# Kernel optimization log

Hardware: AMD Instinct MI355X
Metric: run time of the kernel (lower is better)

## Reference

```python
import jax, jax.numpy as jnp
import numpy as np

DIM = 1024
NUM_HEADS = 16
HEAD_DIM = DIM // NUM_HEADS
SCALE = HEAD_DIM ** -0.5
B, N = 2, 2048


def setup_inputs() -> dict:
    key = jax.random.key(0)
    k_x, k_qkv, k_prjw, k_prjb = jax.random.split(key, 4)
    # nn.Linear(dim, 3*dim, bias=False): weight [3*dim, dim]
    s = 1.0 / np.sqrt(DIM)
    return {
        "x": jax.random.normal(k_x, (B, N, DIM), dtype=jnp.float32),
        "w_qkv": jax.random.uniform(k_qkv, (3 * DIM, DIM), jnp.float32, -s, s),
        "w_prj": jax.random.uniform(k_prjw, (DIM, DIM), jnp.float32, -s, s),
        "b_prj": jax.random.uniform(k_prjb, (DIM,), jnp.float32, -s, s),
    }


def reference(x, w_qkv, w_prj, b_prj):
    Bb, Nn, C = x.shape
    qkv = jnp.einsum("bnc,dc->bnd", x, w_qkv)            # [B,N,3C]
    qkv = qkv.reshape(Bb, Nn, 3, NUM_HEADS, HEAD_DIM)
    qkv = jnp.transpose(qkv, (2, 0, 3, 1, 4))            # [3,B,H,N,hd]
    q, k, v = qkv[0], qkv[1], qkv[2]
    attn = jnp.einsum("bhqd,bhkd->bhqk", q, k) * SCALE   # [B,H,N,N]
    attn = jax.nn.softmax(attn, axis=-1)
    out = jnp.einsum("bhqk,bhkd->bhqd", attn, v)         # [B,H,N,hd]
    out = jnp.transpose(out, (0, 2, 1, 3)).reshape(Bb, Nn, C)
    # dropout layers are identity at eval / p=0
    return jnp.einsum("bnc,dc->bnd", out, w_prj) + b_prj
```

## Files before the change

### kernel.cpp

```cpp
#include <hip/hip_runtime.h>

typedef unsigned short u16;
typedef unsigned int u32;
typedef __attribute__((ext_vector_type(8))) short s16x8;
typedef __attribute__((ext_vector_type(4))) short s16x4;
typedef __attribute__((ext_vector_type(4))) float f32x4;

#define DIM    1024
#define NHEADS 16
#define HD     64
#define NSEQ   2048
#define QKVN   3072

__device__ __forceinline__ u16 f2bf(float f) {
  u32 u = __float_as_uint(f);
  u += 0x7FFF + ((u >> 16) & 1);
  return (u16)(u >> 16);
}

__device__ __forceinline__ float vexp2(float x) {
#if __has_builtin(__builtin_amdgcn_exp2f)
  return __builtin_amdgcn_exp2f(x);
#else
  return __expf(x * 0.69314718055994531f);
#endif
}

__device__ __forceinline__ void async16(const u16* g, u16* l) {
  __builtin_amdgcn_global_load_lds(
      (const __attribute__((address_space(1))) unsigned int*)g,
      (__attribute__((address_space(3))) unsigned int*)l, 16, 0, 0);
}

__global__ void cast_all(const float* __restrict__ x, const float* __restrict__ wq,
                         const float* __restrict__ wp, u16* __restrict__ xo,
                         u16* __restrict__ wqo, u16* __restrict__ wpo) {
  int i = blockIdx.x * 256 + threadIdx.x;
  const float4* src; u16* dst; int off;
  if (i < 1048576)      { src = (const float4*)x;  dst = xo;  off = i; }
  else if (i < 1835008) { src = (const float4*)wq; dst = wqo; off = i - 1048576; }
  else                  { src = (const float4*)wp; dst = wpo; off = i - 1835008; }
  float4 f = src[off];
  ushort4 o;
  o.x = f2bf(f.x); o.y = f2bf(f.y); o.z = f2bf(f.z); o.w = f2bf(f.w);
  ((ushort4*)dst)[off] = o;
}

template <bool FINAL>
__global__ __launch_bounds__(256, 3) void gemm_bt(
    const u16* __restrict__ A, const u16* __restrict__ Bw, u16* __restrict__ qkv,
    u16* __restrict__ vt, const float* __restrict__ bias, float* __restrict__ outp) {
  constexpr int K = 1024;
  constexpr int BM = FINAL ? 64 : 128;
  constexpr int MT = FINAL ? 64 : 32;
  constexpr int IT = FINAL ? 2 : 4;
  constexpr int ACALLS = BM / 16;
  constexpr int TCALLS = ACALLS + 8;
  constexpr int PW = TCALLS / 4;
  const int bm = blockIdx.x % MT;
  const int bn = blockIdx.x / MT;
  const int tid = threadIdx.x;
  const int wave = tid >> 6, lane = tid & 63;
  const int q4 = lane >> 4, l15 = lane & 15;
  const int wm = wave >> 1, wn = wave & 1;
  const int m0 = bm * BM, n0 = bn * 128;

  __shared__ alignas(16) u16 lsA[BM * 32];
  __shared__ alignas(16) u16 lsB[128 * 32];

  f32x4 acc[IT][4];
#pragma unroll
  for (int i = 0; i < IT; i++)
#pragma unroll
    for (int j = 0; j < 4; j++) acc[i][j] = (f32x4){0.f, 0.f, 0.f, 0.f};

  for (int k0 = 0; k0 < K; k0 += 32) {
    __syncthreads();
#pragma unroll
    for (int j = 0; j < PW; ++j) {
      int t = wave * PW + j;
      if (t < ACALLS) {
        int lin = t * 64 + lane;
        int r = lin >> 2, c = lin & 3;
        async16(A + (size_t)(m0 + r) * K + k0 + c * 8, lsA + t * 512);
      } else {
        int tb = t - ACALLS;
        int lin = tb * 64 + lane;
        int r = lin >> 2, c = lin & 3;
        async16(Bw + (size_t)(n0 + r) * K + k0 + c * 8, lsB + tb * 512);
      }
    }
    __syncthreads();
    s16x8 af[IT], bfr[4];
#pragma unroll
    for (int i = 0; i < IT; ++i)
      af[i] = *(const s16x8*)(lsA + (wm * (IT * 16) + i * 16 + l15) * 32 + q4 * 8);
#pragma unroll
    for (int j = 0; j < 4; ++j)
      bfr[j] = *(const s16x8*)(lsB + (wn * 64 + j * 16 + l15) * 32 + q4 * 8);
#pragma unroll
    for (int i = 0; i < IT; ++i)
#pragma unroll
      for (int j = 0; j < 4; ++j)
        acc[i][j] = __builtin_amdgcn_mfma_f32_16x16x32_bf16(af[i], bfr[j], acc[i][j], 0, 0, 0);
  }

#pragma unroll
  for (int i = 0; i < IT; i++) {
#pragma unroll
    for (int j = 0; j < 4; j++) {
      int n = n0 + wn * 64 + j * 16 + l15;
      int mb = m0 + wm * (IT * 16) + i * 16 + q4 * 4;
      if (FINAL) {
#pragma unroll
        for (int r = 0; r < 4; r++)
          outp[(size_t)(mb + r) * DIM + n] = acc[i][j][r] + bias[n];
      } else if (n < 2048) {
#pragma unroll
        for (int r = 0; r < 4; r++)
          qkv[(size_t)(mb + r) * QKVN + n] = f2bf(acc[i][j][r]);
      } else {
        int b = mb >> 11, tok = mb & 2047;
        int h = (n >> 6) & 15, hd = n & 63;
        ushort4 pk;
        pk.x = f2bf(acc[i][j][0]); pk.y = f2bf(acc[i][j][1]);
        pk.z = f2bf(acc[i][j][2]); pk.w = f2bf(acc[i][j][3]);
        *(ushort4*)(vt + ((size_t)((b * NHEADS + h) * HD + hd)) * NSEQ + tok) = pk;
      }
    }
  }
}

__global__ __launch_bounds__(256, 2) void attn_kernel(const u16* __restrict__ qkv,
                                                      const u16* __restrict__ vt,
                                                      u16* __restrict__ aout) {
  const int blk = blockIdx.x;
  const int bh = blk & 31, qt = blk >> 5;
  const int b = bh >> 4, h = bh & 15;
  const int tid = threadIdx.x;
  const int wave = tid >> 6, lane = tid & 63;
  const int g = wave >> 1, wq = wave & 1;
  const int q4 = lane >> 4, l15 = lane & 15;

  __shared__ alignas(16) u16 smem[32768];
  u16* lsKb = smem + g * 2 * 4096;
  u16* lsVb = smem + 16384 + g * 2 * 4096;
  float* lsO = (float*)smem;
  float* lsS = lsO + 64 * 132;

  const float QSCALE = 0.18033688011112042f;
  s16x8 aq[4][2];
#pragma unroll
  for (int rt = 0; rt < 4; ++rt)
#pragma unroll
    for (int kc = 0; kc < 2; ++kc) {
      int row = b * NSEQ + qt * 128 + wq * 64 + rt * 16 + l15;
      uint4 d = *(const uint4*)(qkv + (size_t)row * QKVN + h * HD + kc * 32 + q4 * 8);
      u32 w[4] = {d.x, d.y, d.z, d.w};
      s16x8 f;
#pragma unroll
      for (int j = 0; j < 8; ++j) {
        u16 u = (u16)(w[j >> 1] >> ((j & 1) * 16));
        float v = __uint_as_float(((u32)u) << 16) * QSCALE;
        f[j] = (short)f2bf(v);
      }
      aq[rt][kc] = f;
    }

  f32x4 o[4][4];
  float lsum[4] = {0.f, 0.f, 0.f, 0.f};
#pragma unroll
  for (int rt = 0; rt < 4; ++rt)
#pragma unroll
    for (int ht = 0; ht < 4; ++ht) o[rt][ht] = (f32x4){0.f, 0.f, 0.f, 0.f};

  auto stage = [&](int ktl, int buf) {
#pragma unroll
    for (int j = 0; j < 4; ++j) {
      int t = wq * 4 + j;
      int lin = t * 64 + lane;
      int r = lin >> 3, c = (lin & 7) ^ (r & 7);
      int key = g * 1024 + ktl * 64;
      async16(qkv + (size_t)(b * NSEQ + key + r) * QKVN + DIM + h * HD + c * 8,
              lsKb + buf * 4096 + t * 512);
      async16(vt + (size_t)(bh * HD + r) * NSEQ + key + c * 8,
              lsVb + buf * 4096 + t * 512);
    }
  };

  stage(0, 0);

  for (int kt = 0; kt < 16; ++kt) {
    const int buf = kt & 1;
    __syncthreads();
    if (kt + 1 < 16) stage(kt + 1, buf ^ 1);
    const u16* lsK = lsKb + buf * 4096;
    const u16* lsV = lsVb + buf * 4096;

    s16x8 kf[2][4];
#pragma unroll
    for (int kc = 0; kc < 2; ++kc)
#pragma unroll
      for (int ct = 0; ct < 4; ++ct) {
        int r = ct * 16 + l15;
        int c = (kc * 4 + q4) ^ (r & 7);
        kf[kc][ct] = *(const s16x8*)(lsK + r * 64 + c * 8);
      }
    s16x4 vf[4][4];
#pragma unroll
    for (int ct = 0; ct < 4; ++ct)
#pragma unroll
      for (int ht = 0; ht < 4; ++ht) {
        int row = ht * 16 + l15;
        int gch = ct * 2 + (q4 >> 1);
        int p = gch ^ (row & 7);
        vf[ct][ht] = *(const s16x4*)(lsV + row * 64 + p * 8 + (q4 & 1) * 4);
      }

#pragma unroll
    for (int rt = 0; rt < 4; ++rt) {
      f32x4 st[4];
#pragma unroll
      for (int ct = 0; ct < 4; ++ct) st[ct] = (f32x4){0.f, 0.f, 0.f, 0.f};
#pragma unroll
      for (int kc = 0; kc < 2; ++kc)
#pragma unroll
        for (int ct = 0; ct < 4; ++ct)
          st[ct] = __builtin_amdgcn_mfma_f32_16x16x32_bf16(kf[kc][ct], aq[rt][kc], st[ct], 0, 0, 0);

      s16x4 pa[4];
#pragma unroll
      for (int ct = 0; ct < 4; ++ct) {
        u32 u0 = __float_as_uint(vexp2(st[ct][0]));
        u32 u1 = __float_as_uint(vexp2(st[ct][1]));
        u32 u2 = __float_as_uint(vexp2(st[ct][2]));
        u32 u3 = __float_as_uint(vexp2(st[ct][3]));
        lsum[rt] += __uint_as_float(u0 & 0xffff0000u) + __uint_as_float(u1 & 0xffff0000u) +
                    __uint_as_float(u2 & 0xffff0000u) + __uint_as_float(u3 & 0xffff0000u);
        union { u32 w[2]; s16x4 v; } pk;
        pk.w[0] = (u0 >> 16) | (u1 & 0xffff0000u);
        pk.w[1] = (u2 >> 16) | (u3 & 0xffff0000u);
        pa[ct] = pk.v;
      }

#pragma unroll
      for (int ct = 0; ct < 4; ++ct)
#pragma unroll
        for (int ht = 0; ht < 4; ++ht)
          o[rt][ht] = __builtin_amdgcn_mfma_f32_16x16x16bf16_1k(pa[ct], vf[ct][ht], o[rt][ht], 0, 0, 0);
    }
  }

#pragma unroll
  for (int rt = 0; rt < 4; ++rt) {
    lsum[rt] += __shfl_xor(lsum[rt], 16, 64);
    lsum[rt] += __shfl_xor(lsum[rt], 32, 64);
  }

  __syncthreads();
  if (g == 1) {
#pragma unroll
    for (int rt = 0; rt < 4; ++rt) {
#pragma unroll
      for (int ht = 0; ht < 4; ++ht) {
        int addr = (ht * 16 + l15) * 132 + wq * 64 + rt * 16 + q4 * 4;
        *(float4*)(lsO + addr) = (float4){o[rt][ht][0], o[rt][ht][1], o[rt][ht][2], o[rt][ht][3]};
      }
      if (q4 == 0) lsS[wq * 64 + rt * 16 + l15] = lsum[rt];
    }
  }
  __syncthreads();
  if (g == 0) {
#pragma unroll
    for (int rt = 0; rt < 4; ++rt) {
      float4 s2 = *(const float4*)(lsS + wq * 64 + rt * 16 + q4 * 4);
      float inv[4];
      inv[0] = 1.0f / (__shfl(lsum[rt], q4 * 4 + 0, 64) + s2.x);
      inv[1] = 1.0f / (__shfl(lsum[rt], q4 * 4 + 1, 64) + s2.y);
      inv[2] = 1.0f / (__shfl(lsum[rt], q4 * 4 + 2, 64) + s2.z);
      inv[3] = 1.0f / (__shfl(lsum[rt], q4 * 4 + 3, 64) + s2.w);
#pragma unroll
      for (int ht = 0; ht < 4; ++ht) {
        float4 o2 = *(const float4*)(lsO + (ht * 16 + l15) * 132 + wq * 64 + rt * 16 + q4 * 4);
        float v[4] = {o[rt][ht][0] + o2.x, o[rt][ht][1] + o2.y,
                      o[rt][ht][2] + o2.z, o[rt][ht][3] + o2.w};
#pragma unroll
        for (int r = 0; r < 4; ++r) {
          int n = qt * 128 + wq * 64 + rt * 16 + q4 * 4 + r;
          int col = h * HD + ht * 16 + l15;
          aout[(size_t)(b * NSEQ + n) * DIM + col] = f2bf(v[r] * inv[r]);
        }
      }
    }
  }
}

extern "C" void kernel_launch(void* const* d_in, const int* in_sizes, int n_in,
                              void* d_out, int out_size, void* d_ws, size_t ws_size,
                              hipStream_t stream) {
  const float* x     = (const float*)d_in[0];
  const float* w_qkv = (const float*)d_in[1];
  const float* w_prj = (const float*)d_in[2];
  const float* b_prj = (const float*)d_in[3];
  float* out = (float*)d_out;

  char* ws = (char*)d_ws;
  u16* x_bf    = (u16*)(ws);
  u16* wqkv_bf = (u16*)(ws + (size_t)(8u << 20));
  u16* wprj_bf = (u16*)(ws + (size_t)(14u << 20));
  u16* qkv     = (u16*)(ws + (size_t)(16u << 20));
  u16* vt      = (u16*)(ws + (size_t)(40u << 20));
  u16* aout    = (u16*)(ws + (size_t)(48u << 20));

  cast_all<<<8192, 256, 0, stream>>>(x, w_qkv, w_prj, x_bf, wqkv_bf, wprj_bf);
  gemm_bt<false><<<32 * 24, 256, 0, stream>>>(x_bf, wqkv_bf, qkv, vt, nullptr, nullptr);
  attn_kernel<<<512, 256, 0, stream>>>(qkv, vt, aout);
  gemm_bt<true><<<64 * 8, 256, 0, stream>>>(aout, wprj_bf, nullptr, nullptr, b_prj, out);
}
```

Measured before the change: 180.4 us.

## Double-buffer GEMM LDS tiles, compute softmax row sums via MFMA, add setprio

The projection GEMM now double-buffers its LDS tiles, so the global-to-LDS copy of the next K slice overlaps the MFMAs on the current one, with a single barrier per iteration. In attention, the softmax denominator is accumulated by an extra MFMA against a ones vector instead of scalar adds plus cross-lane shuffles, which removes VALU work and the final reduction. s_setprio hints are placed around the MFMA blocks in both kernels. The trade is doubled GEMM LDS use, which may hurt occupancy at 3 blocks per CU, plus one extra MFMA per P tile.

```diff
diff --git a/kernel.cpp b/kernel.cpp
--- a/kernel.cpp
+++ b/kernel.cpp
@@ -65,8 +65,8 @@
   const int wm = wave >> 1, wn = wave & 1;
   const int m0 = bm * BM, n0 = bn * 128;
 
-  __shared__ alignas(16) u16 lsA[BM * 32];
-  __shared__ alignas(16) u16 lsB[128 * 32];
+  __shared__ alignas(16) u16 lsA[2][BM * 32];
+  __shared__ alignas(16) u16 lsB[2][128 * 32];
 
   f32x4 acc[IT][4];
 #pragma unroll
@@ -74,35 +74,43 @@
 #pragma unroll
     for (int j = 0; j < 4; j++) acc[i][j] = (f32x4){0.f, 0.f, 0.f, 0.f};
 
-  for (int k0 = 0; k0 < K; k0 += 32) {
-    __syncthreads();
+  auto stage = [&](int k0, int buf) {
 #pragma unroll
     for (int j = 0; j < PW; ++j) {
       int t = wave * PW + j;
       if (t < ACALLS) {
         int lin = t * 64 + lane;
         int r = lin >> 2, c = lin & 3;
-        async16(A + (size_t)(m0 + r) * K + k0 + c * 8, lsA + t * 512);
+        async16(A + (size_t)(m0 + r) * K + k0 + c * 8, lsA[buf] + t * 512);
       } else {
         int tb = t - ACALLS;
         int lin = tb * 64 + lane;
         int r = lin >> 2, c = lin & 3;
-        async16(Bw + (size_t)(n0 + r) * K + k0 + c * 8, lsB + tb * 512);
-      }
-    }
+        async16(Bw + (size_t)(n0 + r) * K + k0 + c * 8, lsB[buf] + tb * 512);
+      }
+    }
+  };
+
+  stage(0, 0);
+
+  for (int k0 = 0; k0 < K; k0 += 32) {
+    const int buf = (k0 >> 5) & 1;
     __syncthreads();
+    if (k0 + 32 < K) stage(k0 + 32, buf ^ 1);
     s16x8 af[IT], bfr[4];
 #pragma unroll
     for (int i = 0; i < IT; ++i)
-      af[i] = *(const s16x8*)(lsA + (wm * (IT * 16) + i * 16 + l15) * 32 + q4 * 8);
+      af[i] = *(const s16x8*)(lsA[buf] + (wm * (IT * 16) + i * 16 + l15) * 32 + q4 * 8);
 #pragma unroll
     for (int j = 0; j < 4; ++j)
-      bfr[j] = *(const s16x8*)(lsB + (wn * 64 + j * 16 + l15) * 32 + q4 * 8);
+      bfr[j] = *(const s16x8*)(lsB[buf] + (wn * 64 + j * 16 + l15) * 32 + q4 * 8);
+    __builtin_amdgcn_s_setprio(1);
 #pragma unroll
     for (int i = 0; i < IT; ++i)
 #pragma unroll
       for (int j = 0; j < 4; ++j)
         acc[i][j] = __builtin_amdgcn_mfma_f32_16x16x32_bf16(af[i], bfr[j], acc[i][j], 0, 0, 0);
+    __builtin_amdgcn_s_setprio(0);
   }
 
 #pragma unroll
@@ -168,11 +176,14 @@
     }
 
   f32x4 o[4][4];
-  float lsum[4] = {0.f, 0.f, 0.f, 0.f};
-#pragma unroll
-  for (int rt = 0; rt < 4; ++rt)
+  f32x4 osum[4];
+  const s16x4 vones = {(short)0x3F80, (short)0x3F80, (short)0x3F80, (short)0x3F80};
+#pragma unroll
+  for (int rt = 0; rt < 4; ++rt) {
+    osum[rt] = (f32x4){0.f, 0.f, 0.f, 0.f};
 #pragma unroll
     for (int ht = 0; ht < 4; ++ht) o[rt][ht] = (f32x4){0.f, 0.f, 0.f, 0.f};
+  }
 
   auto stage = [&](int ktl, int buf) {
 #pragma unroll
@@ -222,11 +233,13 @@
       f32x4 st[4];
 #pragma unroll
       for (int ct = 0; ct < 4; ++ct) st[ct] = (f32x4){0.f, 0.f, 0.f, 0.f};
+      __builtin_amdgcn_s_setprio(1);
 #pragma unroll
       for (int kc = 0; kc < 2; ++kc)
 #pragma unroll
         for (int ct = 0; ct < 4; ++ct)
           st[ct] = __builtin_amdgcn_mfma_f32_16x16x32_bf16(kf[kc][ct], aq[rt][kc], st[ct], 0, 0, 0);
+      __builtin_amdgcn_s_setprio(0);
 
       s16x4 pa[4];
 #pragma unroll
@@ -235,26 +248,22 @@
         u32 u1 = __float_as_uint(vexp2(st[ct][1]));
         u32 u2 = __float_as_uint(vexp2(st[ct][2]));
         u32 u3 = __float_as_uint(vexp2(st[ct][3]));
-        lsum[rt] += __uint_as_float(u0 & 0xffff0000u) + __uint_as_float(u1 & 0xffff0000u) +
-                    __uint_as_float(u2 & 0xffff0000u) + __uint_as_float(u3 & 0xffff0000u);
         union { u32 w[2]; s16x4 v; } pk;
         pk.w[0] = (u0 >> 16) | (u1 & 0xffff0000u);
         pk.w[1] = (u2 >> 16) | (u3 & 0xffff0000u);
         pa[ct] = pk.v;
       }
 
-#pragma unroll
-      for (int ct = 0; ct < 4; ++ct)
+      __builtin_amdgcn_s_setprio(1);
+#pragma unroll
+      for (int ct = 0; ct < 4; ++ct) {
+        osum[rt] = __builtin_amdgcn_mfma_f32_16x16x16bf16_1k(pa[ct], vones, osum[rt], 0, 0, 0);
 #pragma unroll
         for (int ht = 0; ht < 4; ++ht)
           o[rt][ht] = __builtin_amdgcn_mfma_f32_16x16x16bf16_1k(pa[ct], vf[ct][ht], o[rt][ht], 0, 0, 0);
-    }
-  }
-
-#pragma unroll
-  for (int rt = 0; rt < 4; ++rt) {
-    lsum[rt] += __shfl_xor(lsum[rt], 16, 64);
-    lsum[rt] += __shfl_xor(lsum[rt], 32, 64);
+      }
+      __builtin_amdgcn_s_setprio(0);
+    }
   }
 
   __syncthreads();
@@ -266,7 +275,11 @@
         int addr = (ht * 16 + l15) * 132 + wq * 64 + rt * 16 + q4 * 4;
         *(float4*)(lsO + addr) = (float4){o[rt][ht][0], o[rt][ht][1], o[rt][ht][2], o[rt][ht][3]};
       }
-      if (q4 == 0) lsS[wq * 64 + rt * 16 + l15] = lsum[rt];
+      if (l15 == 0) {
+#pragma unroll
+        for (int r = 0; r < 4; ++r)
+          lsS[wq * 64 + rt * 16 + q4 * 4 + r] = osum[rt][r];
+      }
     }
   }
   __syncthreads();
@@ -275,10 +288,10 @@
     for (int rt = 0; rt < 4; ++rt) {
       float4 s2 = *(const float4*)(lsS + wq * 64 + rt * 16 + q4 * 4);
       float inv[4];
-      inv[0] = 1.0f / (__shfl(lsum[rt], q4 * 4 + 0, 64) + s2.x);
-      inv[1] = 1.0f / (__shfl(lsum[rt], q4 * 4 + 1, 64) + s2.y);
-      inv[2] = 1.0f / (__shfl(lsum[rt], q4 * 4 + 2, 64) + s2.z);
-      inv[3] = 1.0f / (__shfl(lsum[rt], q4 * 4 + 3, 64) + s2.w);
+      inv[0] = 1.0f / (osum[rt][0] + s2.x);
+      inv[1] = 1.0f / (osum[rt][1] + s2.y);
+      inv[2] = 1.0f / (osum[rt][2] + s2.z);
+      inv[3] = 1.0f / (osum[rt][3] + s2.w);
 #pragma unroll
       for (int ht = 0; ht < 4; ++ht) {
         float4 o2 = *(const float4*)(lsO + (ht * 16 + l15) * 132 + wq * 64 + rt * 16 + q4 * 4);
```

Result: no change. 178.4 us (-1.1%).
